# Performance work log

Hardware: AMD Instinct MI355X
Metric: run time of the kernel (lower is better)

Reference implementation:

```python
import jax, jax.numpy as jnp
import numpy as np

B, T = 512, 16384


def ema(x, alpha):
    """Row-wise EMA: y_0 = x_0, y_t = alpha*x_t + (1-alpha)*y_{t-1}. x: [B, T]."""
    one_minus = 1.0 - alpha

    def step(carry, xt):  # carry: [B], xt: [B]
        y = alpha * xt + one_minus * carry
        return y, y

    init = x[:, 0]
    _, ys = jax.lax.scan(step, init, x[:, 1:].T)  # ys: [T-1, B]
    return jnp.concatenate([x[:, :1], ys.T], axis=1)  # [B, T]


def setup_inputs() -> dict:
    key = jax.random.key(0)
    data = jax.random.normal(key, (B, T), dtype=jnp.float32)
    return {"data": data, "short_period": 12, "long_period": 26, "signal_period": 9}


def reference(data, short_period, long_period, signal_period):
    short_alpha = 2.0 / (short_period + 1)
    long_alpha = 2.0 / (long_period + 1)
    signal_alpha = 2.0 / (signal_period + 1)
    macd_line = ema(data, short_alpha) - ema(data, long_alpha)
    signal_line = ema(macd_line, signal_alpha)
    hist = macd_line - signal_line
    return (macd_line, signal_line, hist)
```

## Files before the change

### kernel.cpp

```cpp
#include <hip/hip_runtime.h>


constexpr int kB = 512;
constexpr int kT = 16384;
constexpr int kSeg = 1024;
constexpr int kChunk = 256;
constexpr int kChunks = 5;
constexpr int kSegsPerRow = kT / kSeg;
constexpr int kWPB = 4;

template <int STEPS>
__device__ __forceinline__ void wave_scan(float agg, float m0, int lane,
                                          float& ex, float& tot) {
  float m = m0, z = agg;
#pragma unroll
  for (int i = 0; i < STEPS; ++i) {
    const int d = 1 << i;
    float t = __shfl_up(z, d, 64);
    if (lane >= d) z = fmaf(m, t, z);
    m = m * m;
  }
  ex = __shfl_up(z, 1, 64);
  if (lane == 0) ex = 0.0f;
  tot = __shfl(z, 63, 64);
}

__device__ __forceinline__ float pow4lane(float b4, int lane) {
  float m = b4, pw = 1.0f;
#pragma unroll
  for (int i = 0; i < 6; ++i) {
    if (lane & (1 << i)) pw *= m;
    m = m * m;
  }
  return pw;
}

__global__ __launch_bounds__(kWPB * 64, 4)
void macd_kernel(const float* __restrict__ x,
                 const int* __restrict__ p_short,
                 const int* __restrict__ p_long,
                 const int* __restrict__ p_sig,
                 float* __restrict__ out) {
  const int lane = threadIdx.x & 63;
  const int wid  = (blockIdx.x * blockDim.x + threadIdx.x) >> 6;
  const int row  = wid >> 4;
  const int seg  = wid & (kSegsPerRow - 1);
  const int p0   = seg * kSeg - kChunk;

  const float a_s = 2.0f / (float)(p_short[0] + 1), b_s = 1.0f - a_s;
  const float a_l = 2.0f / (float)(p_long[0]  + 1), b_l = 1.0f - a_l;
  const float a_g = 2.0f / (float)(p_sig[0]   + 1), b_g = 1.0f - a_g;
  const float b2_s = b_s * b_s, b4_s = b2_s * b2_s;
  const float b2_l = b_l * b_l, b4_l = b2_l * b2_l;
  const float b2_g = b_g * b_g, b4_g = b2_g * b2_g;
  const float pw_s = pow4lane(b4_s, lane);
  const float pw_l = pow4lane(b4_l, lane);
  const float pw_g = pow4lane(b4_g, lane);

  const float* xr = x + row * kT;

  float4 xq[kChunks];
  if (p0 >= 0) {
#pragma unroll
    for (int k = 0; k < kChunks; ++k)
      xq[k] = *(const float4*)(xr + p0 + k * kChunk + lane * 4);
  } else {
    const float x0v = xr[0];
    xq[0] = make_float4(x0v, x0v, x0v, x0v);
#pragma unroll
    for (int k = 1; k < kChunks; ++k)
      xq[k] = *(const float4*)(xr + p0 + k * kChunk + lane * 4);
  }
  const float xfirst = __shfl(xq[0].x, 0, 64);

  float ls[kChunks][4], ll[kChunks][4];
  float exs[kChunks], Ts[kChunks], exl[kChunks], Tl[kChunks];
#pragma unroll
  for (int k = 0; k < kChunks; ++k) {
    ls[k][0] = a_s * xq[k].x;
    ls[k][1] = fmaf(b_s, ls[k][0], a_s * xq[k].y);
    ls[k][2] = fmaf(b_s, ls[k][1], a_s * xq[k].z);
    ls[k][3] = fmaf(b_s, ls[k][2], a_s * xq[k].w);
    ll[k][0] = a_l * xq[k].x;
    ll[k][1] = fmaf(b_l, ll[k][0], a_l * xq[k].y);
    ll[k][2] = fmaf(b_l, ll[k][1], a_l * xq[k].z);
    ll[k][3] = fmaf(b_l, ll[k][2], a_l * xq[k].w);
    wave_scan<4>(ls[k][3], b4_s, lane, exs[k], Ts[k]);
    wave_scan<5>(ll[k][3], b4_l, lane, exl[k], Tl[k]);
  }

  float m[kChunks][4];
  float lg[kChunks][4];
  float exg[kChunks], Tg[kChunks];
#pragma unroll
  for (int k = 0; k < kChunks; ++k) {
    const float Cs = (k == 0) ? xfirst : Ts[k - 1];
    const float Cl = (k == 0) ? xfirst : Tl[k - 1];
    const float cin_s = fmaf(pw_s, Cs, exs[k]);
    const float cin_l = fmaf(pw_l, Cl, exl[k]);
    m[k][0] = fmaf(b_s, cin_s, ls[k][0]) - fmaf(b_l, cin_l, ll[k][0]);
    m[k][1] = fmaf(b2_s, cin_s, ls[k][1]) - fmaf(b2_l, cin_l, ll[k][1]);
    m[k][2] = fmaf(b2_s * b_s, cin_s, ls[k][2]) - fmaf(b2_l * b_l, cin_l, ll[k][2]);
    m[k][3] = fmaf(b4_s, cin_s, ls[k][3]) - fmaf(b4_l, cin_l, ll[k][3]);
    lg[k][0] = a_g * m[k][0];
    lg[k][1] = fmaf(b_g, lg[k][0], a_g * m[k][1]);
    lg[k][2] = fmaf(b_g, lg[k][1], a_g * m[k][2]);
    lg[k][3] = fmaf(b_g, lg[k][2], a_g * m[k][3]);
    wave_scan<4>(lg[k][3], b4_g, lane, exg[k], Tg[k]);
  }

  float* om = out + row * kT;
  float* og = om + kB * kT;
  float* oh = og + kB * kT;

#pragma unroll
  for (int k = 1; k < kChunks; ++k) {
    const float Cg = Tg[k - 1];
    const float cin_g = fmaf(pw_g, Cg, exg[k]);
    float4 mv, gv, hv;
    mv.x = m[k][0]; mv.y = m[k][1]; mv.z = m[k][2]; mv.w = m[k][3];
    gv.x = fmaf(b_g, cin_g, lg[k][0]);
    gv.y = fmaf(b2_g, cin_g, lg[k][1]);
    gv.z = fmaf(b2_g * b_g, cin_g, lg[k][2]);
    gv.w = fmaf(b4_g, cin_g, lg[k][3]);
    hv.x = mv.x - gv.x; hv.y = mv.y - gv.y;
    hv.z = mv.z - gv.z; hv.w = mv.w - gv.w;
    const int pos = p0 + k * kChunk + lane * 4;
    *(float4*)(om + pos) = mv;
    *(float4*)(og + pos) = gv;
    *(float4*)(oh + pos) = hv;
  }
}

extern "C" void kernel_launch(void* const* d_in, const int* in_sizes, int n_in,
                              void* d_out, int out_size, void* d_ws, size_t ws_size,
                              hipStream_t stream) {
  const float* x = (const float*)d_in[0];
  const int* ps  = (const int*)d_in[1];
  const int* pl  = (const int*)d_in[2];
  const int* pg  = (const int*)d_in[3];
  float* out     = (float*)d_out;

  const int total_waves = kB * kSegsPerRow;
  const int blocks = total_waves / kWPB;
  macd_kernel<<<blocks, kWPB * 64, 0, stream>>>(x, ps, pl, pg, out);
}
```

Before: 132.4 us.

## Express signal EMA as linear combination of three independent input EMAs

Uses partial fractions to write the signal line (an EMA of the difference of two EMAs) as a weighted sum of three EMAs of the raw input, with decay factors b_s, b_l and b_g. This removes the sequential dependency in which the signal scan had to wait for the MACD line, so all three wave scans run in one fused loop with a running carry and fewer live registers. The cost is one extra EMA scan on the input and possible numerical loss when the decay factors are close, because of the divisions by (b_s - b_g) and related terms. Warm-up behaviour in the 256-element halo may also differ from the nested form.

```diff
diff --git a/kernel.cpp b/kernel.cpp
--- a/kernel.cpp
+++ b/kernel.cpp
@@ -50,9 +50,12 @@
   const float a_s = 2.0f / (float)(p_short[0] + 1), b_s = 1.0f - a_s;
   const float a_l = 2.0f / (float)(p_long[0]  + 1), b_l = 1.0f - a_l;
   const float a_g = 2.0f / (float)(p_sig[0]   + 1), b_g = 1.0f - a_g;
-  const float b2_s = b_s * b_s, b4_s = b2_s * b2_s;
-  const float b2_l = b_l * b_l, b4_l = b2_l * b2_l;
-  const float b2_g = b_g * b_g, b4_g = b2_g * b2_g;
+  const float b2_s = b_s * b_s, b3_s = b2_s * b_s, b4_s = b2_s * b2_s;
+  const float b2_l = b_l * b_l, b3_l = b2_l * b_l, b4_l = b2_l * b2_l;
+  const float b2_g = b_g * b_g, b3_g = b2_g * b_g, b4_g = b2_g * b2_g;
+  const float c_s =  a_g * b_s / (b_s - b_g);
+  const float c_l = -a_g * b_l / (b_l - b_g);
+  const float c_g =  b_g * (a_s / (b_g - b_s) - a_l / (b_g - b_l));
   const float pw_s = pow4lane(b4_s, lane);
   const float pw_l = pow4lane(b4_l, lane);
   const float pw_g = pow4lane(b4_g, lane);
@@ -73,62 +76,65 @@
   }
   const float xfirst = __shfl(xq[0].x, 0, 64);
 
-  float ls[kChunks][4], ll[kChunks][4];
-  float exs[kChunks], Ts[kChunks], exl[kChunks], Tl[kChunks];
-#pragma unroll
-  for (int k = 0; k < kChunks; ++k) {
-    ls[k][0] = a_s * xq[k].x;
-    ls[k][1] = fmaf(b_s, ls[k][0], a_s * xq[k].y);
-    ls[k][2] = fmaf(b_s, ls[k][1], a_s * xq[k].z);
-    ls[k][3] = fmaf(b_s, ls[k][2], a_s * xq[k].w);
-    ll[k][0] = a_l * xq[k].x;
-    ll[k][1] = fmaf(b_l, ll[k][0], a_l * xq[k].y);
-    ll[k][2] = fmaf(b_l, ll[k][1], a_l * xq[k].z);
-    ll[k][3] = fmaf(b_l, ll[k][2], a_l * xq[k].w);
-    wave_scan<4>(ls[k][3], b4_s, lane, exs[k], Ts[k]);
-    wave_scan<5>(ll[k][3], b4_l, lane, exl[k], Tl[k]);
-  }
-
-  float m[kChunks][4];
-  float lg[kChunks][4];
-  float exg[kChunks], Tg[kChunks];
-#pragma unroll
-  for (int k = 0; k < kChunks; ++k) {
-    const float Cs = (k == 0) ? xfirst : Ts[k - 1];
-    const float Cl = (k == 0) ? xfirst : Tl[k - 1];
-    const float cin_s = fmaf(pw_s, Cs, exs[k]);
-    const float cin_l = fmaf(pw_l, Cl, exl[k]);
-    m[k][0] = fmaf(b_s, cin_s, ls[k][0]) - fmaf(b_l, cin_l, ll[k][0]);
-    m[k][1] = fmaf(b2_s, cin_s, ls[k][1]) - fmaf(b2_l, cin_l, ll[k][1]);
-    m[k][2] = fmaf(b2_s * b_s, cin_s, ls[k][2]) - fmaf(b2_l * b_l, cin_l, ll[k][2]);
-    m[k][3] = fmaf(b4_s, cin_s, ls[k][3]) - fmaf(b4_l, cin_l, ll[k][3]);
-    lg[k][0] = a_g * m[k][0];
-    lg[k][1] = fmaf(b_g, lg[k][0], a_g * m[k][1]);
-    lg[k][2] = fmaf(b_g, lg[k][1], a_g * m[k][2]);
-    lg[k][3] = fmaf(b_g, lg[k][2], a_g * m[k][3]);
-    wave_scan<4>(lg[k][3], b4_g, lane, exg[k], Tg[k]);
-  }
-
   float* om = out + row * kT;
   float* og = om + kB * kT;
   float* oh = og + kB * kT;
 
+  float Cs = xfirst, Cl = xfirst, Cg = xfirst;
+
 #pragma unroll
-  for (int k = 1; k < kChunks; ++k) {
-    const float Cg = Tg[k - 1];
-    const float cin_g = fmaf(pw_g, Cg, exg[k]);
-    float4 mv, gv, hv;
-    mv.x = m[k][0]; mv.y = m[k][1]; mv.z = m[k][2]; mv.w = m[k][3];
-    gv.x = fmaf(b_g, cin_g, lg[k][0]);
-    gv.y = fmaf(b2_g, cin_g, lg[k][1]);
-    gv.z = fmaf(b2_g * b_g, cin_g, lg[k][2]);
-    gv.w = fmaf(b4_g, cin_g, lg[k][3]);
-    hv.x = mv.x - gv.x; hv.y = mv.y - gv.y;
-    hv.z = mv.z - gv.z; hv.w = mv.w - gv.w;
-    const int pos = p0 + k * kChunk + lane * 4;
-    *(float4*)(om + pos) = mv;
-    *(float4*)(og + pos) = gv;
-    *(float4*)(oh + pos) = hv;
+  for (int k = 0; k < kChunks; ++k) {
+    const float4 xv = xq[k];
+    float s0 = a_s * xv.x;
+    float s1 = fmaf(b_s, s0, a_s * xv.y);
+    float s2 = fmaf(b_s, s1, a_s * xv.z);
+    float s3 = fmaf(b_s, s2, a_s * xv.w);
+    float l0 = a_l * xv.x;
+    float l1 = fmaf(b_l, l0, a_l * xv.y);
+    float l2 = fmaf(b_l, l1, a_l * xv.z);
+    float l3 = fmaf(b_l, l2, a_l * xv.w);
+    float g0 = a_g * xv.x;
+    float g1 = fmaf(b_g, g0, a_g * xv.y);
+    float g2 = fmaf(b_g, g1, a_g * xv.z);
+    float g3 = fmaf(b_g, g2, a_g * xv.w);
+
+    float exs, Ts, exl, Tl, exg, Tg;
+    wave_scan<4>(s3, b4_s, lane, exs, Ts);
+    wave_scan<5>(l3, b4_l, lane, exl, Tl);
+    wave_scan<4>(g3, b4_g, lane, exg, Tg);
+
+    if (k > 0) {
+      const float cin_s = fmaf(pw_s, Cs, exs);
+      const float cin_l = fmaf(pw_l, Cl, exl);
+      const float cin_g = fmaf(pw_g, Cg, exg);
+      const float S0 = fmaf(b_s,  cin_s, s0);
+      const float S1 = fmaf(b2_s, cin_s, s1);
+      const float S2 = fmaf(b3_s, cin_s, s2);
+      const float S3 = fmaf(b4_s, cin_s, s3);
+      const float L0 = fmaf(b_l,  cin_l, l0);
+      const float L1 = fmaf(b2_l, cin_l, l1);
+      const float L2 = fmaf(b3_l, cin_l, l2);
+      const float L3 = fmaf(b4_l, cin_l, l3);
+      const float G0 = fmaf(b_g,  cin_g, g0);
+      const float G1 = fmaf(b2_g, cin_g, g1);
+      const float G2 = fmaf(b3_g, cin_g, g2);
+      const float G3 = fmaf(b4_g, cin_g, g3);
+
+      float4 mv, sv, hv;
+      mv.x = S0 - L0; mv.y = S1 - L1; mv.z = S2 - L2; mv.w = S3 - L3;
+      sv.x = fmaf(c_g, G0, fmaf(c_l, L0, c_s * S0));
+      sv.y = fmaf(c_g, G1, fmaf(c_l, L1, c_s * S1));
+      sv.z = fmaf(c_g, G2, fmaf(c_l, L2, c_s * S2));
+      sv.w = fmaf(c_g, G3, fmaf(c_l, L3, c_s * S3));
+      hv.x = mv.x - sv.x; hv.y = mv.y - sv.y;
+      hv.z = mv.z - sv.z; hv.w = mv.w - sv.w;
+
+      const int pos = p0 + k * kChunk + lane * 4;
+      *(float4*)(om + pos) = mv;
+      *(float4*)(og + pos) = sv;
+      *(float4*)(oh + pos) = hv;
+    }
+    Cs = Ts; Cl = Tl; Cg = Tg;
   }
 }
 
```

Result: no change. 133.5 us (+0.8%).
